# Optimization experiments

Hardware: AMD Instinct MI355X
Metric: run time of the kernel (lower is better)

The kernel has to match this reference:

```python
import jax, jax.numpy as jnp
import numpy as np

DIM = 2048
RATE = 4
LAYER_ID = 0
DYNAMIC_SCALE = 0.01
EPS = 1e-5


def setup_inputs() -> dict:
    key = jax.random.key(0)
    k1, k2, k3, k4 = jax.random.split(key, 4)
    b, l = 2, 4096
    h = jax.random.normal(k1, (b, l, RATE, DIM), dtype=jnp.float32)
    h_o = jax.random.normal(k2, (b, l, DIM), dtype=jnp.float32)
    # LayerNorm affine params
    ln_gamma = jnp.ones((DIM,), dtype=jnp.float32)
    ln_beta = jnp.zeros((DIM,), dtype=jnp.float32)
    # dynamic fns: init to zeros in module; use small random so math is nontrivial
    dynamic_alpha_fn = 0.02 * jax.random.normal(k3, (DIM, RATE + 1), dtype=jnp.float32)
    dynamic_beta_fn = 0.02 * jax.random.normal(k4, (DIM,), dtype=jnp.float32)
    # static alpha: [init_alpha0 | eye(rate)] -> (rate, rate+1)
    init_alpha0 = np.zeros((RATE, 1), dtype=np.float32)
    init_alpha0[LAYER_ID % RATE, 0] = 1.0
    static_alpha = jnp.asarray(np.concatenate([init_alpha0, np.eye(RATE, dtype=np.float32)], axis=1))
    static_beta = jnp.ones((RATE,), dtype=jnp.float32)
    return {
        "h": h,
        "h_o": h_o,
        "ln_gamma": ln_gamma,
        "ln_beta": ln_beta,
        "dynamic_alpha_fn": dynamic_alpha_fn,
        "dynamic_beta_fn": dynamic_beta_fn,
        "static_alpha": static_alpha,
        "static_beta": static_beta,
    }


def _layernorm(x, gamma, beta):
    mu = jnp.mean(x, axis=-1, keepdims=True)
    var = jnp.mean(jnp.square(x - mu), axis=-1, keepdims=True)
    return (x - mu) * jax.lax.rsqrt(var + EPS) * gamma + beta


def reference(h, h_o, ln_gamma, ln_beta, dynamic_alpha_fn, dynamic_beta_fn, static_alpha, static_beta):
    # h: (b, l, n=rate, d); h_o: (b, l, d)
    norm_h = _layernorm(h, ln_gamma, ln_beta)
    # dynamic alpha: (b,l,n,rate+1)
    dyn_alpha = jnp.einsum("blnd,dk->blnk", norm_h, dynamic_alpha_fn) * DYNAMIC_SCALE
    alpha = dyn_alpha + static_alpha[None, None, :, :]  # (b,l,n,k)
    # mix: alpha^T @ h over n -> (b,l,k,d)
    mix_h = jnp.einsum("blnk,blnd->blkd", alpha, h)
    # dynamic beta: (b,l,n)
    dyn_beta = jnp.einsum("blnd,d->bln", norm_h, dynamic_beta_fn) * DYNAMIC_SCALE
    beta = dyn_beta + static_beta[None, None, :]  # (b,l,rate)
    # depth connection: broadcast residual-branch output over rate streams
    out = h_o[:, :, None, :] * beta[..., None] + mix_h[..., 1:, :]
    return out
```

## Files before the change

kernel.cpp:

```cpp
#include <hip/hip_runtime.h>


#define NDIM   2048
#define NRATE  4
#define DSCALE 0.01f
#define LEPS   1e-5f

__global__ __launch_bounds__(256) void hc_fused(
    const float* __restrict__ h,
    const float* __restrict__ h_o,
    const float* __restrict__ g_,
    const float* __restrict__ b_,
    const float* __restrict__ Afn,
    const float* __restrict__ Bfn,
    const float* __restrict__ sA,
    const float* __restrict__ sB,
    float* __restrict__ out)
{
    __shared__ float s_red[4][20];
    __shared__ float s_bc[20];

    const int t    = threadIdx.x;
    const int lane = t & 63;
    const int wave = t >> 6;
    const size_t pbase = (size_t)blockIdx.x * (NRATE * NDIM);
    const int dbase = t * 8;

    float hv[NRATE][8];
    float vals[8];
    #pragma unroll
    for (int n = 0; n < NRATE; n++) {
        const float4 r0 = *(const float4*)(h + pbase + n * NDIM + dbase);
        const float4 r1 = *(const float4*)(h + pbase + n * NDIM + dbase + 4);
        hv[n][0] = r0.x; hv[n][1] = r0.y; hv[n][2] = r0.z; hv[n][3] = r0.w;
        hv[n][4] = r1.x; hv[n][5] = r1.y; hv[n][6] = r1.z; hv[n][7] = r1.w;
        float s = 0.f, ss = 0.f;
        #pragma unroll
        for (int i = 0; i < 8; i++) { s += hv[n][i]; ss = fmaf(hv[n][i], hv[n][i], ss); }
        vals[2 * n]     = s;
        vals[2 * n + 1] = ss;
    }
    #pragma unroll
    for (int i = 0; i < 8; i++) {
        float v = vals[i];
        #pragma unroll
        for (int off = 32; off; off >>= 1) v += __shfl_down(v, off, 64);
        if (lane == 0) s_red[wave][i] = v;
    }
    __syncthreads();
    if (t < 8) s_bc[t] = s_red[0][t] + s_red[1][t] + s_red[2][t] + s_red[3][t];
    __syncthreads();

    float mean[NRATE], rstd[NRATE];
    #pragma unroll
    for (int n = 0; n < NRATE; n++) {
        float m   = s_bc[2 * n] * (1.0f / NDIM);
        float var = s_bc[2 * n + 1] * (1.0f / NDIM) - m * m;
        mean[n] = m;
        rstd[n] = rsqrtf(var + LEPS);
    }

    float pav[20];
    #pragma unroll
    for (int i = 0; i < 20; i++) pav[i] = 0.f;
    #pragma unroll
    for (int i = 0; i < 8; i++) {
        const int d = dbase + i;
        const float gvi  = g_[d];
        const float bvi  = b_[d];
        const float dbvi = Bfn[d];
        const float a0 = Afn[d * 5 + 1];
        const float a1 = Afn[d * 5 + 2];
        const float a2 = Afn[d * 5 + 3];
        const float a3 = Afn[d * 5 + 4];
        #pragma unroll
        for (int n = 0; n < NRATE; n++) {
            const float nh = fmaf((hv[n][i] - mean[n]) * rstd[n], gvi, bvi);
            pav[n * 4 + 0] = fmaf(nh, a0, pav[n * 4 + 0]);
            pav[n * 4 + 1] = fmaf(nh, a1, pav[n * 4 + 1]);
            pav[n * 4 + 2] = fmaf(nh, a2, pav[n * 4 + 2]);
            pav[n * 4 + 3] = fmaf(nh, a3, pav[n * 4 + 3]);
            pav[16 + n]    = fmaf(nh, dbvi, pav[16 + n]);
        }
    }
    #pragma unroll
    for (int i = 0; i < 20; i++) {
        float v = pav[i];
        #pragma unroll
        for (int off = 32; off; off >>= 1) v += __shfl_down(v, off, 64);
        if (lane == 0) s_red[wave][i] = v;
    }
    __syncthreads();
    if (t < 20) s_bc[t] = s_red[0][t] + s_red[1][t] + s_red[2][t] + s_red[3][t];
    __syncthreads();

    float alpha_f[NRATE][4], beta_f[NRATE];
    #pragma unroll
    for (int n = 0; n < NRATE; n++) {
        #pragma unroll
        for (int k = 0; k < 4; k++)
            alpha_f[n][k] = fmaf(DSCALE, s_bc[n * 4 + k], sA[n * 5 + 1 + k]);
        beta_f[n] = fmaf(DSCALE, s_bc[16 + n], sB[n]);
    }

    const float4 ro0 = *(const float4*)(h_o + (size_t)blockIdx.x * NDIM + dbase);
    const float4 ro1 = *(const float4*)(h_o + (size_t)blockIdx.x * NDIM + dbase + 4);
    float ho[8];
    ho[0] = ro0.x; ho[1] = ro0.y; ho[2] = ro0.z; ho[3] = ro0.w;
    ho[4] = ro1.x; ho[5] = ro1.y; ho[6] = ro1.z; ho[7] = ro1.w;

    #pragma unroll
    for (int j = 0; j < NRATE; j++) {
        float o[8];
        #pragma unroll
        for (int i = 0; i < 8; i++) {
            float acc = ho[i] * beta_f[j];
            #pragma unroll
            for (int n = 0; n < NRATE; n++) acc = fmaf(alpha_f[n][j], hv[n][i], acc);
            o[i] = acc;
        }
        float4 w0 = make_float4(o[0], o[1], o[2], o[3]);
        float4 w1 = make_float4(o[4], o[5], o[6], o[7]);
        *(float4*)(out + pbase + j * NDIM + dbase)     = w0;
        *(float4*)(out + pbase + j * NDIM + dbase + 4) = w1;
    }
}

extern "C" void kernel_launch(void* const* d_in, const int* in_sizes, int n_in,
                              void* d_out, int out_size, void* d_ws, size_t ws_size,
                              hipStream_t stream) {
    const float* h   = (const float*)d_in[0];
    const float* h_o = (const float*)d_in[1];
    const float* g   = (const float*)d_in[2];
    const float* b   = (const float*)d_in[3];
    const float* A   = (const float*)d_in[4];
    const float* Bf  = (const float*)d_in[5];
    const float* sA  = (const float*)d_in[6];
    const float* sB  = (const float*)d_in[7];
    float* out = (float*)d_out;

    const int P = in_sizes[1] / NDIM;
    hc_fused<<<P, 256, 0, stream>>>(h, h_o, g, b, A, Bf, sA, sB, out);
}
```

Before: 490.5 us.

## Fold LayerNorm into single-pass projection sums with precomputed weight products

The LayerNorm-then-project computation is rewritten so the projections are expanded algebraically. Raw sums, sums of squares and gamma-weighted projections of x are gathered in one pass, then corrected with mean and rstd. This removes the second reduction round and one barrier pair. A small prep kernel packs gamma, beta_fn and alpha_fn into a workspace and precomputes the gamma·A and beta·A dot products, which adds a launch. The change also swaps shuffle reductions for DPP row operations, interleaves thread column chunks for coalescing, and uses nontemporal output stores; the expanded form may lose some precision to cancellation.

```diff
diff --git a/kernel.cpp b/kernel.cpp
--- a/kernel.cpp
+++ b/kernel.cpp
@@ -6,105 +6,155 @@
 #define DSCALE 0.01f
 #define LEPS   1e-5f
 
-__global__ __launch_bounds__(256) void hc_fused(
+typedef float vfloat4 __attribute__((ext_vector_type(4)));
+
+#define WS_PK2 16
+#define WS_PK4 4112
+
+template <int C>
+__device__ __forceinline__ float dppmv(float x) {
+    return __builtin_bit_cast(float,
+        __builtin_amdgcn_update_dpp(0, __builtin_bit_cast(int, x), C, 0xF, 0xF, true));
+}
+
+__device__ __forceinline__ float wsum(float x) {
+    x += dppmv<0x111>(x);
+    x += dppmv<0x112>(x);
+    x += dppmv<0x114>(x);
+    x += dppmv<0x118>(x);
+    x += dppmv<0x142>(x);
+    x += dppmv<0x143>(x);
+    return x;
+}
+
+__global__ __launch_bounds__(256) void hc_prep(
+    const float* __restrict__ g_, const float* __restrict__ b_,
+    const float* __restrict__ Afn, const float* __restrict__ Bfn,
+    float* __restrict__ ws)
+{
+    __shared__ float s_red[4][10];
+    const int t = threadIdx.x;
+    const int lane = t & 63, wave = t >> 6;
+    float acc[10];
+    #pragma unroll
+    for (int v = 0; v < 10; v++) acc[v] = 0.f;
+    #pragma unroll
+    for (int i = 0; i < 8; i++) {
+        const int d = t * 8 + i;
+        const float g  = g_[d];
+        const float b  = b_[d];
+        const float db = Bfn[d];
+        const float a1 = Afn[d*5+1], a2 = Afn[d*5+2], a3 = Afn[d*5+3], a4 = Afn[d*5+4];
+        *(float2*)(ws + WS_PK2 + 2*d) = make_float2(g, db);
+        *(float4*)(ws + WS_PK4 + 4*d) = make_float4(a1, a2, a3, a4);
+        acc[0] = fmaf(g, a1, acc[0]); acc[1] = fmaf(g, a2, acc[1]);
+        acc[2] = fmaf(g, a3, acc[2]); acc[3] = fmaf(g, a4, acc[3]);
+        acc[4] = fmaf(b, a1, acc[4]); acc[5] = fmaf(b, a2, acc[5]);
+        acc[6] = fmaf(b, a3, acc[6]); acc[7] = fmaf(b, a4, acc[7]);
+        acc[8] = fmaf(g, db, acc[8]); acc[9] = fmaf(b, db, acc[9]);
+    }
+    #pragma unroll
+    for (int v = 0; v < 10; v++) {
+        float w = wsum(acc[v]);
+        if (lane == 63) s_red[wave][v] = w;
+    }
+    __syncthreads();
+    if (t < 10) ws[t] = s_red[0][t] + s_red[1][t] + s_red[2][t] + s_red[3][t];
+}
+
+__global__ __launch_bounds__(256) void hc_main(
     const float* __restrict__ h,
     const float* __restrict__ h_o,
-    const float* __restrict__ g_,
-    const float* __restrict__ b_,
-    const float* __restrict__ Afn,
-    const float* __restrict__ Bfn,
     const float* __restrict__ sA,
     const float* __restrict__ sB,
+    const float* __restrict__ ws,
     float* __restrict__ out)
 {
-    __shared__ float s_red[4][20];
-    __shared__ float s_bc[20];
+    __shared__ float s_red[4][28];
+    __shared__ float s_bc[28];
 
     const int t    = threadIdx.x;
     const int lane = t & 63;
     const int wave = t >> 6;
     const size_t pbase = (size_t)blockIdx.x * (NRATE * NDIM);
-    const int dbase = t * 8;
+    const int dc0 = 4 * t;
+    const int dc1 = 1024 + 4 * t;
 
     float hv[NRATE][8];
-    float vals[8];
     #pragma unroll
     for (int n = 0; n < NRATE; n++) {
-        const float4 r0 = *(const float4*)(h + pbase + n * NDIM + dbase);
-        const float4 r1 = *(const float4*)(h + pbase + n * NDIM + dbase + 4);
+        const float4 r0 = *(const float4*)(h + pbase + n * NDIM + dc0);
+        const float4 r1 = *(const float4*)(h + pbase + n * NDIM + dc1);
         hv[n][0] = r0.x; hv[n][1] = r0.y; hv[n][2] = r0.z; hv[n][3] = r0.w;
         hv[n][4] = r1.x; hv[n][5] = r1.y; hv[n][6] = r1.z; hv[n][7] = r1.w;
-        float s = 0.f, ss = 0.f;
+    }
+    const float4 ro0 = *(const float4*)(h_o + (size_t)blockIdx.x * NDIM + dc0);
+    const float4 ro1 = *(const float4*)(h_o + (size_t)blockIdx.x * NDIM + dc1);
+
+    const float GA0 = ws[0], GA1 = ws[1], GA2 = ws[2], GA3 = ws[3];
+    const float BA0 = ws[4], BA1 = ws[5], BA2 = ws[6], BA3 = ws[7];
+    const float GB  = ws[8], BB  = ws[9];
+
+    float S[NRATE]  = {0.f, 0.f, 0.f, 0.f};
+    float SS[NRATE] = {0.f, 0.f, 0.f, 0.f};
+    float Q[NRATE]  = {0.f, 0.f, 0.f, 0.f};
+    float Pk[NRATE][4] = {};
+    #pragma unroll
+    for (int c = 0; c < 2; c++) {
+        const int dc = c ? dc1 : dc0;
         #pragma unroll
-        for (int i = 0; i < 8; i++) { s += hv[n][i]; ss = fmaf(hv[n][i], hv[n][i], ss); }
-        vals[2 * n]     = s;
-        vals[2 * n + 1] = ss;
+        for (int i = 0; i < 4; i++) {
+            const int d = dc + i;
+            const float2 gb = *(const float2*)(ws + WS_PK2 + 2 * d);
+            const float4 a  = *(const float4*)(ws + WS_PK4 + 4 * d);
+            #pragma unroll
+            for (int n = 0; n < NRATE; n++) {
+                const float x = hv[n][c * 4 + i];
+                S[n] += x;
+                SS[n] = fmaf(x, x, SS[n]);
+                const float xg = x * gb.x;
+                Pk[n][0] = fmaf(xg, a.x, Pk[n][0]);
+                Pk[n][1] = fmaf(xg, a.y, Pk[n][1]);
+                Pk[n][2] = fmaf(xg, a.z, Pk[n][2]);
+                Pk[n][3] = fmaf(xg, a.w, Pk[n][3]);
+                Q[n]     = fmaf(xg, gb.y, Q[n]);
+            }
+        }
+    }
+
+    float red[28];
+    #pragma unroll
+    for (int n = 0; n < NRATE; n++) {
+        red[n]     = S[n];
+        red[4 + n] = SS[n];
+        red[8 + n] = Q[n];
+        #pragma unroll
+        for (int k = 0; k < 4; k++) red[12 + n * 4 + k] = Pk[n][k];
     }
     #pragma unroll
-    for (int i = 0; i < 8; i++) {
-        float v = vals[i];
-        #pragma unroll
-        for (int off = 32; off; off >>= 1) v += __shfl_down(v, off, 64);
-        if (lane == 0) s_red[wave][i] = v;
+    for (int v = 0; v < 28; v++) {
+        float w = wsum(red[v]);
+        if (lane == 63) s_red[wave][v] = w;
     }
     __syncthreads();
-    if (t < 8) s_bc[t] = s_red[0][t] + s_red[1][t] + s_red[2][t] + s_red[3][t];
-    __syncthreads();
-
-    float mean[NRATE], rstd[NRATE];
-    #pragma unroll
-    for (int n = 0; n < NRATE; n++) {
-        float m   = s_bc[2 * n] * (1.0f / NDIM);
-        float var = s_bc[2 * n + 1] * (1.0f / NDIM) - m * m;
-        mean[n] = m;
-        rstd[n] = rsqrtf(var + LEPS);
-    }
-
-    float pav[20];
-    #pragma unroll
-    for (int i = 0; i < 20; i++) pav[i] = 0.f;
-    #pragma unroll
-    for (int i = 0; i < 8; i++) {
-        const int d = dbase + i;
-        const float gvi  = g_[d];
-        const float bvi  = b_[d];
-        const float dbvi = Bfn[d];
-        const float a0 = Afn[d * 5 + 1];
-        const float a1 = Afn[d * 5 + 2];
-        const float a2 = Afn[d * 5 + 3];
-        const float a3 = Afn[d * 5 + 4];
-        #pragma unroll
-        for (int n = 0; n < NRATE; n++) {
-            const float nh = fmaf((hv[n][i] - mean[n]) * rstd[n], gvi, bvi);
-            pav[n * 4 + 0] = fmaf(nh, a0, pav[n * 4 + 0]);
-            pav[n * 4 + 1] = fmaf(nh, a1, pav[n * 4 + 1]);
-            pav[n * 4 + 2] = fmaf(nh, a2, pav[n * 4 + 2]);
-            pav[n * 4 + 3] = fmaf(nh, a3, pav[n * 4 + 3]);
-            pav[16 + n]    = fmaf(nh, dbvi, pav[16 + n]);
-        }
-    }
-    #pragma unroll
-    for (int i = 0; i < 20; i++) {
-        float v = pav[i];
-        #pragma unroll
-        for (int off = 32; off; off >>= 1) v += __shfl_down(v, off, 64);
-        if (lane == 0) s_red[wave][i] = v;
-    }
-    __syncthreads();
-    if (t < 20) s_bc[t] = s_red[0][t] + s_red[1][t] + s_red[2][t] + s_red[3][t];
+    if (t < 28) s_bc[t] = s_red[0][t] + s_red[1][t] + s_red[2][t] + s_red[3][t];
     __syncthreads();
 
     float alpha_f[NRATE][4], beta_f[NRATE];
     #pragma unroll
     for (int n = 0; n < NRATE; n++) {
-        #pragma unroll
-        for (int k = 0; k < 4; k++)
-            alpha_f[n][k] = fmaf(DSCALE, s_bc[n * 4 + k], sA[n * 5 + 1 + k]);
-        beta_f[n] = fmaf(DSCALE, s_bc[16 + n], sB[n]);
+        const float m   = s_bc[n] * (1.0f / NDIM);
+        const float var = s_bc[4 + n] * (1.0f / NDIM) - m * m;
+        const float rs  = rsqrtf(var + LEPS);
+        const float p0 = s_bc[12 + n * 4 + 0], p1 = s_bc[12 + n * 4 + 1];
+        const float p2 = s_bc[12 + n * 4 + 2], p3 = s_bc[12 + n * 4 + 3];
+        alpha_f[n][0] = fmaf(DSCALE, fmaf(rs, fmaf(-m, GA0, p0), BA0), sA[n * 5 + 1]);
+        alpha_f[n][1] = fmaf(DSCALE, fmaf(rs, fmaf(-m, GA1, p1), BA1), sA[n * 5 + 2]);
+        alpha_f[n][2] = fmaf(DSCALE, fmaf(rs, fmaf(-m, GA2, p2), BA2), sA[n * 5 + 3]);
+        alpha_f[n][3] = fmaf(DSCALE, fmaf(rs, fmaf(-m, GA3, p3), BA3), sA[n * 5 + 4]);
+        beta_f[n]     = fmaf(DSCALE, fmaf(rs, fmaf(-m, GB, s_bc[8 + n]), BB), sB[n]);
     }
 
-    const float4 ro0 = *(const float4*)(h_o + (size_t)blockIdx.x * NDIM + dbase);
-    const float4 ro1 = *(const float4*)(h_o + (size_t)blockIdx.x * NDIM + dbase + 4);
     float ho[8];
     ho[0] = ro0.x; ho[1] = ro0.y; ho[2] = ro0.z; ho[3] = ro0.w;
     ho[4] = ro1.x; ho[5] = ro1.y; ho[6] = ro1.z; ho[7] = ro1.w;
@@ -119,10 +169,10 @@
             for (int n = 0; n < NRATE; n++) acc = fmaf(alpha_f[n][j], hv[n][i], acc);
             o[i] = acc;
         }
-        float4 w0 = make_float4(o[0], o[1], o[2], o[3]);
-        float4 w1 = make_float4(o[4], o[5], o[6], o[7]);
-        *(float4*)(out + pbase + j * NDIM + dbase)     = w0;
-        *(float4*)(out + pbase + j * NDIM + dbase + 4) = w1;
+        vfloat4 w0 = { o[0], o[1], o[2], o[3] };
+        vfloat4 w1 = { o[4], o[5], o[6], o[7] };
+        __builtin_nontemporal_store(w0, (vfloat4*)(out + pbase + j * NDIM + dc0));
+        __builtin_nontemporal_store(w1, (vfloat4*)(out + pbase + j * NDIM + dc1));
     }
 }
 
@@ -138,7 +188,9 @@
     const float* sA  = (const float*)d_in[6];
     const float* sB  = (const float*)d_in[7];
     float* out = (float*)d_out;
+    float* ws  = (float*)d_ws;
 
     const int P = in_sizes[1] / NDIM;
-    hc_fused<<<P, 256, 0, stream>>>(h, h_o, g, b, A, Bf, sA, sB, out);
+    hc_prep<<<1, 256, 0, stream>>>(g, b, A, Bf, ws);
+    hc_main<<<P, 256, 0, stream>>>(h, h_o, sA, sB, ws, out);
 }
```

Measured after the change: 490.2 us. No clear change (-0.1%).
